# Performance work log

Hardware: AMD Instinct MI355X
Metric: run time of the kernel (lower is better)

## Reference

```python
import jax, jax.numpy as jnp
import numpy as np

N = 20000      # nodes
E = 200000     # edges
IN = 128       # in_feat
OUT = 128      # out_feat
NB = 8         # num_bases
SI = IN // NB  # submat_in = 16
SO = OUT // NB # submat_out = 16
R = 230        # num_rels
T = 365        # total_times


def setup_inputs() -> dict:
    key = jax.random.key(0)
    ks = jax.random.split(key, 11)
    h = jax.random.normal(ks[0], (N, IN), jnp.float32)
    edge_norm = jax.random.uniform(ks[1], (E, 1), jnp.float32)
    node_norm = jax.random.uniform(ks[2], (N, 1), jnp.float32)
    weight = jax.random.normal(ks[3], (R, NB * SI * SO), jnp.float32) * 0.05
    h_bias = jnp.zeros((OUT,), jnp.float32)
    loop_weight = jax.random.normal(ks[4], (IN, OUT), jnp.float32) * 0.05
    time_embed = jax.random.normal(ks[5], (T, IN), jnp.float32) * 0.05
    edge_src = jax.random.randint(ks[6], (E,), 0, N)
    edge_dst = jax.random.randint(ks[7], (E,), 0, N)
    edge_type = jax.random.randint(ks[8], (E,), 0, R)
    time_idx = jax.random.randint(ks[9], (N,), 0, T)
    return dict(h=h, edge_norm=edge_norm, node_norm=node_norm, weight=weight,
                h_bias=h_bias, loop_weight=loop_weight, time_embed=time_embed,
                edge_src=edge_src, edge_dst=edge_dst, edge_type=edge_type,
                time_idx=time_idx)


def reference(h, edge_norm, node_norm, weight, h_bias, loop_weight, time_embed,
              edge_src, edge_dst, edge_type, time_idx):
    # self-loop message
    loop_message = h @ loop_weight                              # [N, OUT]
    # msg_func: per-edge relation weight gather + block-diagonal bmm
    W_e = weight[edge_type].reshape(-1, NB, SI, SO)             # [E, NB, SI, SO]
    src = h[edge_src].reshape(-1, NB, SI)                       # [E, NB, SI]
    msg = jnp.einsum('ebi,ebio->ebo', src, W_e).reshape(-1, OUT)  # [E, OUT]
    msg = msg * edge_norm
    # fn.sum aggregation over destination nodes
    agg = jax.ops.segment_sum(msg, edge_dst, num_segments=N)    # [N, OUT]
    # apply_func: scale by node norm, then bias + self loop + activation
    node_repr = agg * node_norm
    node_repr = node_repr + h_bias + loop_message
    node_repr = jax.nn.relu(node_repr)
    # get_time_embedding: per-node time embedding gather
    time_embedding = time_embed[time_idx]                       # [N, IN]
    return node_repr, time_embedding
```

## Files before the change

kernel.cpp:

```cpp
#include <hip/hip_runtime.h>

#define N 20000
#define E 200000
#define IN 128
#define OUT 128
#define NB 8
#define SI 16
#define SO 16
#define R 230
#define T 365

__device__ float  g_W_t[(size_t)R * NB * SO * SI];
__device__ ushort g_msg[(size_t)E * OUT];
__device__ int    g_cnt_d[N];
__device__ int    g_off_d[N];
__device__ int    g_cur_d[N];
__device__ int    g_cnt_r[R * 16];
__device__ int    g_cur_r[R * 16];
__device__ int    g_pos[E];
__device__ int    g_eid_r[E];
__device__ int    g_total_d;
__device__ int    g_total_r;

__device__ __forceinline__ ushort f2bf(float f) {
    unsigned u = __float_as_uint(f);
    return (ushort)((u + 0x7fffu + ((u >> 16) & 1u)) >> 16);
}
__device__ __forceinline__ float bf2f(ushort v) {
    return __uint_as_float((unsigned)v << 16);
}

__global__ __launch_bounds__(256) void hist_kernel(
        const float* __restrict__ weight,
        const int* __restrict__ edge_dst,
        const int* __restrict__ edge_type) {
    __shared__ int lh[R];
    const int tid  = threadIdx.x;
    const int gtid = blockIdx.x * 256 + tid;
    for (int t = gtid; t < R * NB * SI * SO; t += gridDim.x * 256) {
        int r  = t >> 11;
        int b  = (t >> 8) & 7;
        int ol = (t >> 4) & 15;
        int i  = t & 15;
        g_W_t[t] = weight[(long)r * 2048 + b * 256 + i * 16 + ol];
    }
    for (int j = tid; j < R; j += 256) lh[j] = 0;
    __syncthreads();
    for (long e = gtid; e < E; e += (long)gridDim.x * 256) {
        atomicAdd(&g_cnt_d[edge_dst[e]], 1);
        atomicAdd(&lh[edge_type[e]], 1);
    }
    __syncthreads();
    for (int j = tid; j < R; j += 256)
        if (lh[j]) atomicAdd(&g_cnt_r[j * 16], lh[j]);
}

__global__ __launch_bounds__(256) void alloc_kernel() {
    int idx  = blockIdx.x * blockDim.x + threadIdx.x;
    int lane = threadIdx.x & 63;
    const int NPAD = 20032;
    if (idx < NPAD) {
        int c = (idx < N) ? g_cnt_d[idx] : 0;
        int x = c;
        for (int d = 1; d < 64; d <<= 1) {
            int y = __shfl_up(x, d);
            if (lane >= d) x += y;
        }
        int base = 0;
        if (lane == 63) base = atomicAdd(&g_total_d, x);
        base = __shfl(base, 63);
        if (idx < N) {
            int off = base + x - c;
            g_off_d[idx] = off;
            g_cur_d[idx] = off;
        }
    } else if (idx < NPAD + 256) {
        int j = idx - NPAD;
        int c = (j < R) ? g_cnt_r[j * 16] : 0;
        int x = c;
        for (int d = 1; d < 64; d <<= 1) {
            int y = __shfl_up(x, d);
            if (lane >= d) x += y;
        }
        int base = 0;
        if (lane == 63) base = atomicAdd(&g_total_r, x);
        base = __shfl(base, 63);
        if (j < R) g_cur_r[j * 16] = base + x - c;
    }
}

__global__ void scatter_kernel(const int* __restrict__ edge_dst,
                               const int* __restrict__ edge_type) {
    int e = blockIdx.x * blockDim.x + threadIdx.x;
    if (e < E) {
        g_pos[e] = atomicAdd(&g_cur_d[edge_dst[e]], 1);
        int pr = atomicAdd(&g_cur_r[edge_type[e] * 16], 1);
        g_eid_r[pr] = e;
    }
}

__global__ __launch_bounds__(256) void msg_kernel(
        const float* __restrict__ h,
        const float* __restrict__ edge_norm,
        const int* __restrict__ edge_src,
        const int* __restrict__ edge_type) {
    __shared__ __attribute__((aligned(16))) float hsm[32 * 132];
    __shared__ int   ssrc[32], stype[32], spos[32];
    __shared__ float snorm[32];

    const int tid = threadIdx.x;
    const int lo  = blockIdx.x * 32;

    if (tid < 32) {
        int e = g_eid_r[lo + tid];
        ssrc[tid]  = edge_src[e];
        stype[tid] = edge_type[e];
        snorm[tid] = edge_norm[e];
        spos[tid]  = g_pos[e];
    }
    __syncthreads();

    {
        const int row = tid >> 3;
        const int c0  = (tid & 7) * 4;
        const float* hp = h + (long)ssrc[row] * IN;
        float* dst = &hsm[row * 132];
#pragma unroll
        for (int j = 0; j < 4; ++j) {
            float4 v = *reinterpret_cast<const float4*>(hp + c0 + 32 * j);
            *reinterpret_cast<float4*>(dst + c0 + 32 * j) = v;
        }
    }
    __syncthreads();

    const int slot = tid >> 7;
    const int o    = tid & 127;
    const int b    = o >> 4;
    const int ol   = o & 15;

#define MSG_BODY(K, W0, W1, W2, W3)                                          \
    {                                                                        \
        const float* hrow = &hsm[(K) * 132 + b * 16];                        \
        float4 h0 = *reinterpret_cast<const float4*>(hrow);                  \
        float4 h1 = *reinterpret_cast<const float4*>(hrow + 4);              \
        float4 h2 = *reinterpret_cast<const float4*>(hrow + 8);              \
        float4 h3 = *reinterpret_cast<const float4*>(hrow + 12);             \
        float m0 = 0.f, m1 = 0.f;                                            \
        m0 = fmaf(h0.x, W0.x, m0); m0 = fmaf(h0.y, W0.y, m0);                \
        m0 = fmaf(h0.z, W0.z, m0); m0 = fmaf(h0.w, W0.w, m0);                \
        m1 = fmaf(h1.x, W1.x, m1); m1 = fmaf(h1.y, W1.y, m1);                \
        m1 = fmaf(h1.z, W1.z, m1); m1 = fmaf(h1.w, W1.w, m1);                \
        m0 = fmaf(h2.x, W2.x, m0); m0 = fmaf(h2.y, W2.y, m0);                \
        m0 = fmaf(h2.z, W2.z, m0); m0 = fmaf(h2.w, W2.w, m0);                \
        m1 = fmaf(h3.x, W3.x, m1); m1 = fmaf(h3.y, W3.y, m1);                \
        m1 = fmaf(h3.z, W3.z, m1); m1 = fmaf(h3.w, W3.w, m1);                \
        __builtin_nontemporal_store(f2bf(snorm[K] * (m0 + m1)),              \
                                    &g_msg[(long)spos[K] * OUT + o]);        \
    }

    if (stype[0] == stype[31]) {
        const float4* wp = reinterpret_cast<const float4*>(
            g_W_t + (long)stype[0] * 2048 + b * 256 + ol * 16);
        float4 w0 = wp[0], w1 = wp[1], w2 = wp[2], w3 = wp[3];
#pragma unroll 4
        for (int k = slot; k < 32; k += 2)
            MSG_BODY(k, w0, w1, w2, w3)
    } else {
        int rcur = -1;
        float4 w0, w1, w2, w3;
        for (int k = slot; k < 32; k += 2) {
            int r = stype[k];
            if (r != rcur) {
                const float4* wp = reinterpret_cast<const float4*>(
                    g_W_t + (long)r * 2048 + b * 256 + ol * 16);
                w0 = wp[0]; w1 = wp[1]; w2 = wp[2]; w3 = wp[3];
                rcur = r;
            }
            MSG_BODY(k, w0, w1, w2, w3)
        }
    }
#undef MSG_BODY
}

__global__ __launch_bounds__(128) void node_kernel(
        const float* __restrict__ h,
        const float* __restrict__ node_norm,
        const float* __restrict__ h_bias,
        const float* __restrict__ loop_weight,
        const float* __restrict__ time_embed,
        const int* __restrict__ time_idx,
        float* __restrict__ out) {
    __shared__ float hsm[IN * 8];
    const int o    = threadIdx.x;
    const int base = blockIdx.x * 8;

    for (int k = o; k < 8 * IN; k += 128) {
        int nl = k >> 7;
        int i  = k & 127;
        hsm[i * 8 + nl] = h[(long)(base + nl) * IN + i];
    }
    __syncthreads();

    float acc[8];
#pragma unroll
    for (int nl = 0; nl < 8; ++nl) {
        int n  = base + nl;
        int st = g_off_d[n];
        int cn = g_cnt_d[n];
        float a0 = 0.f, a1 = 0.f, a2 = 0.f, a3 = 0.f;
        const ushort* mp = g_msg + (long)st * OUT + o;
        int k = 0;
        for (; k + 3 < cn; k += 4) {
            a0 += bf2f(__builtin_nontemporal_load(&mp[(long)(k + 0) * OUT]));
            a1 += bf2f(__builtin_nontemporal_load(&mp[(long)(k + 1) * OUT]));
            a2 += bf2f(__builtin_nontemporal_load(&mp[(long)(k + 2) * OUT]));
            a3 += bf2f(__builtin_nontemporal_load(&mp[(long)(k + 3) * OUT]));
        }
        for (; k < cn; ++k)
            a0 += bf2f(__builtin_nontemporal_load(&mp[(long)k * OUT]));
        acc[nl] = ((a0 + a1) + (a2 + a3)) * node_norm[n];
    }

    float sl[8];
#pragma unroll
    for (int nl = 0; nl < 8; ++nl) sl[nl] = 0.f;

    for (int i0 = 0; i0 < IN; i0 += 8) {
        float w[8];
#pragma unroll
        for (int j = 0; j < 8; ++j)
            w[j] = loop_weight[(long)(i0 + j) * OUT + o];
#pragma unroll
        for (int j = 0; j < 8; ++j) {
            const float* row = &hsm[(i0 + j) * 8];
            float4 p0 = *reinterpret_cast<const float4*>(row);
            float4 p1 = *reinterpret_cast<const float4*>(row + 4);
            sl[0] = fmaf(p0.x, w[j], sl[0]); sl[1] = fmaf(p0.y, w[j], sl[1]);
            sl[2] = fmaf(p0.z, w[j], sl[2]); sl[3] = fmaf(p0.w, w[j], sl[3]);
            sl[4] = fmaf(p1.x, w[j], sl[4]); sl[5] = fmaf(p1.y, w[j], sl[5]);
            sl[6] = fmaf(p1.z, w[j], sl[6]); sl[7] = fmaf(p1.w, w[j], sl[7]);
        }
    }

    const float bias = h_bias[o];
#pragma unroll
    for (int nl = 0; nl < 8; ++nl) {
        int n = base + nl;
        float v = acc[nl] + bias + sl[nl];
        out[(long)n * OUT + o] = fmaxf(v, 0.f);
        out[(long)N * OUT + (long)n * IN + o] =
            time_embed[(long)time_idx[n] * IN + o];
    }

    __syncthreads();
    if (o < 8) g_cnt_d[base + o] = 0;
    {
        int j = blockIdx.x * 128 + o;
        if (j < R * 16) g_cnt_r[j] = 0;
    }
    if (blockIdx.x == 0 && o == 0) { g_total_d = 0; g_total_r = 0; }
}

extern "C" void kernel_launch(void* const* d_in, const int* in_sizes, int n_in,
                              void* d_out, int out_size, void* d_ws, size_t ws_size,
                              hipStream_t stream) {
    const float* h           = (const float*)d_in[0];
    const float* edge_norm   = (const float*)d_in[1];
    const float* node_norm   = (const float*)d_in[2];
    const float* weight      = (const float*)d_in[3];
    const float* h_bias      = (const float*)d_in[4];
    const float* loop_weight = (const float*)d_in[5];
    const float* time_embed  = (const float*)d_in[6];
    const int*   edge_src    = (const int*)d_in[7];
    const int*   edge_dst    = (const int*)d_in[8];
    const int*   edge_type   = (const int*)d_in[9];
    const int*   time_idx    = (const int*)d_in[10];
    float* out = (float*)d_out;

    hist_kernel<<<400, 256, 0, stream>>>(weight, edge_dst, edge_type);
    alloc_kernel<<<80, 256, 0, stream>>>();
    scatter_kernel<<<(E + 255) / 256, 256, 0, stream>>>(edge_dst, edge_type);
    msg_kernel<<<E / 32, 256, 0, stream>>>(h, edge_norm, edge_src, edge_type);
    node_kernel<<<N / 8, 128, 0, stream>>>(h, node_norm, h_bias, loop_weight,
                                           time_embed, time_idx, out);
}
```

Baseline: 229.5 us.

## Fuse prefix-scan into histogram kernel via last-block pattern; widen node kernel loads

Merges the alloc kernel into the histogram kernel: the last block to finish, detected with an atomic counter and fences, performs the prefix scans over destination and relation counts, which removes one launch. The node kernel is restructured so each thread handles two output columns, reading bf16 message pairs as 32-bit words and loop_weight as float2. It also reads h rows directly instead of staging them in shared memory, processing 16 nodes per 256-thread block. The serial scan of 20000 counts in a single block may lengthen the critical path, and the g_done counter now has to be reset in the node kernel.

```diff
diff --git a/kernel.cpp b/kernel.cpp
--- a/kernel.cpp
+++ b/kernel.cpp
@@ -21,6 +21,7 @@
 __device__ int    g_eid_r[E];
 __device__ int    g_total_d;
 __device__ int    g_total_r;
+__device__ unsigned g_done;
 
 __device__ __forceinline__ ushort f2bf(float f) {
     unsigned u = __float_as_uint(f);
@@ -29,15 +30,24 @@
 __device__ __forceinline__ float bf2f(ushort v) {
     return __uint_as_float((unsigned)v << 16);
 }
-
-__global__ __launch_bounds__(256) void hist_kernel(
+__device__ __forceinline__ float bflo(unsigned m) {
+    return __uint_as_float(m << 16);
+}
+__device__ __forceinline__ float bfhi(unsigned m) {
+    return __uint_as_float(m & 0xffff0000u);
+}
+
+__global__ __launch_bounds__(256) void build_kernel(
         const float* __restrict__ weight,
         const int* __restrict__ edge_dst,
         const int* __restrict__ edge_type) {
     __shared__ int lh[R];
+    __shared__ int s_last;
     const int tid  = threadIdx.x;
     const int gtid = blockIdx.x * 256 + tid;
-    for (int t = gtid; t < R * NB * SI * SO; t += gridDim.x * 256) {
+    const int GSZ  = gridDim.x * 256;
+
+    for (int t = gtid; t < R * NB * SI * SO; t += GSZ) {
         int r  = t >> 11;
         int b  = (t >> 8) & 7;
         int ol = (t >> 4) & 15;
@@ -46,46 +56,55 @@
     }
     for (int j = tid; j < R; j += 256) lh[j] = 0;
     __syncthreads();
-    for (long e = gtid; e < E; e += (long)gridDim.x * 256) {
+    for (int e = gtid; e < E; e += GSZ) {
         atomicAdd(&g_cnt_d[edge_dst[e]], 1);
         atomicAdd(&lh[edge_type[e]], 1);
     }
     __syncthreads();
     for (int j = tid; j < R; j += 256)
         if (lh[j]) atomicAdd(&g_cnt_r[j * 16], lh[j]);
-}
-
-__global__ __launch_bounds__(256) void alloc_kernel() {
-    int idx  = blockIdx.x * blockDim.x + threadIdx.x;
-    int lane = threadIdx.x & 63;
-    const int NPAD = 20032;
-    if (idx < NPAD) {
-        int c = (idx < N) ? g_cnt_d[idx] : 0;
+
+    __syncthreads();
+    if (tid == 0) {
+        __threadfence();
+        unsigned d = atomicAdd(&g_done, 1u);
+        s_last = (d == (unsigned)(gridDim.x - 1)) ? 1 : 0;
+    }
+    __syncthreads();
+    if (!s_last) return;
+    __threadfence();
+
+    const int lane = tid & 63;
+    for (int idx = tid; idx < 20032; idx += 256) {
+        int c = (idx < N) ? __hip_atomic_load(&g_cnt_d[idx], __ATOMIC_RELAXED,
+                                              __HIP_MEMORY_SCOPE_AGENT) : 0;
         int x = c;
         for (int d = 1; d < 64; d <<= 1) {
             int y = __shfl_up(x, d);
             if (lane >= d) x += y;
         }
-        int base = 0;
-        if (lane == 63) base = atomicAdd(&g_total_d, x);
-        base = __shfl(base, 63);
+        int bse = 0;
+        if (lane == 63) bse = atomicAdd(&g_total_d, x);
+        bse = __shfl(bse, 63);
         if (idx < N) {
-            int off = base + x - c;
+            int off = bse + x - c;
             g_off_d[idx] = off;
             g_cur_d[idx] = off;
         }
-    } else if (idx < NPAD + 256) {
-        int j = idx - NPAD;
-        int c = (j < R) ? g_cnt_r[j * 16] : 0;
+    }
+    {
+        int j = tid;
+        int c = (j < R) ? __hip_atomic_load(&g_cnt_r[j * 16], __ATOMIC_RELAXED,
+                                            __HIP_MEMORY_SCOPE_AGENT) : 0;
         int x = c;
         for (int d = 1; d < 64; d <<= 1) {
             int y = __shfl_up(x, d);
             if (lane >= d) x += y;
         }
-        int base = 0;
-        if (lane == 63) base = atomicAdd(&g_total_r, x);
-        base = __shfl(base, 63);
-        if (j < R) g_cur_r[j * 16] = base + x - c;
+        int bse = 0;
+        if (lane == 63) bse = atomicAdd(&g_total_r, x);
+        bse = __shfl(bse, 63);
+        if (j < R) g_cur_r[j * 16] = bse + x - c;
     }
 }
 
@@ -182,7 +201,7 @@
 #undef MSG_BODY
 }
 
-__global__ __launch_bounds__(128) void node_kernel(
+__global__ __launch_bounds__(256) void node_kernel(
         const float* __restrict__ h,
         const float* __restrict__ node_norm,
         const float* __restrict__ h_bias,
@@ -190,75 +209,101 @@
         const float* __restrict__ time_embed,
         const int* __restrict__ time_idx,
         float* __restrict__ out) {
-    __shared__ float hsm[IN * 8];
-    const int o    = threadIdx.x;
-    const int base = blockIdx.x * 8;
-
-    for (int k = o; k < 8 * IN; k += 128) {
-        int nl = k >> 7;
-        int i  = k & 127;
-        hsm[i * 8 + nl] = h[(long)(base + nl) * IN + i];
-    }
-    __syncthreads();
-
-    float acc[8];
+    const int t    = threadIdx.x;
+    const int q    = t & 63;
+    const int grp  = t >> 6;
+    const int base = blockIdx.x * 16 + grp * 4;
+
+    const unsigned* msg32 = reinterpret_cast<const unsigned*>(g_msg);
+
+    float accL[4], accH[4];
 #pragma unroll
-    for (int nl = 0; nl < 8; ++nl) {
-        int n  = base + nl;
-        int st = g_off_d[n];
-        int cn = g_cnt_d[n];
-        float a0 = 0.f, a1 = 0.f, a2 = 0.f, a3 = 0.f;
-        const ushort* mp = g_msg + (long)st * OUT + o;
+    for (int nl = 0; nl < 4; ++nl) {
+        const int n  = base + nl;
+        const int st = g_off_d[n];
+        const int cn = g_cnt_d[n];
+        const unsigned* mp = msg32 + (size_t)st * 64 + q;
+        float aL0 = 0.f, aL1 = 0.f, aH0 = 0.f, aH1 = 0.f;
         int k = 0;
         for (; k + 3 < cn; k += 4) {
-            a0 += bf2f(__builtin_nontemporal_load(&mp[(long)(k + 0) * OUT]));
-            a1 += bf2f(__builtin_nontemporal_load(&mp[(long)(k + 1) * OUT]));
-            a2 += bf2f(__builtin_nontemporal_load(&mp[(long)(k + 2) * OUT]));
-            a3 += bf2f(__builtin_nontemporal_load(&mp[(long)(k + 3) * OUT]));
-        }
-        for (; k < cn; ++k)
-            a0 += bf2f(__builtin_nontemporal_load(&mp[(long)k * OUT]));
-        acc[nl] = ((a0 + a1) + (a2 + a3)) * node_norm[n];
-    }
-
-    float sl[8];
+            unsigned m0 = __builtin_nontemporal_load(mp + (size_t)(k + 0) * 64);
+            unsigned m1 = __builtin_nontemporal_load(mp + (size_t)(k + 1) * 64);
+            unsigned m2 = __builtin_nontemporal_load(mp + (size_t)(k + 2) * 64);
+            unsigned m3 = __builtin_nontemporal_load(mp + (size_t)(k + 3) * 64);
+            aL0 += bflo(m0); aH0 += bfhi(m0);
+            aL1 += bflo(m1); aH1 += bfhi(m1);
+            aL0 += bflo(m2); aH0 += bfhi(m2);
+            aL1 += bflo(m3); aH1 += bfhi(m3);
+        }
+        for (; k < cn; ++k) {
+            unsigned m = __builtin_nontemporal_load(mp + (size_t)k * 64);
+            aL0 += bflo(m); aH0 += bfhi(m);
+        }
+        float nn = node_norm[n];
+        accL[nl] = (aL0 + aL1) * nn;
+        accH[nl] = (aH0 + aH1) * nn;
+    }
+
+    float slL0 = 0.f, slL1 = 0.f, slL2 = 0.f, slL3 = 0.f;
+    float slH0 = 0.f, slH1 = 0.f, slH2 = 0.f, slH3 = 0.f;
+    const float2* lw2 = reinterpret_cast<const float2*>(loop_weight);
+    const float* hp0 = h + (size_t)(base + 0) * IN;
+    const float* hp1 = h + (size_t)(base + 1) * IN;
+    const float* hp2 = h + (size_t)(base + 2) * IN;
+    const float* hp3 = h + (size_t)(base + 3) * IN;
+#pragma unroll 4
+    for (int i0 = 0; i0 < IN; i0 += 4) {
+        float2 w0 = lw2[(size_t)(i0 + 0) * 64 + q];
+        float2 w1 = lw2[(size_t)(i0 + 1) * 64 + q];
+        float2 w2 = lw2[(size_t)(i0 + 2) * 64 + q];
+        float2 w3 = lw2[(size_t)(i0 + 3) * 64 + q];
+        float4 v0 = *reinterpret_cast<const float4*>(hp0 + i0);
+        float4 v1 = *reinterpret_cast<const float4*>(hp1 + i0);
+        float4 v2 = *reinterpret_cast<const float4*>(hp2 + i0);
+        float4 v3 = *reinterpret_cast<const float4*>(hp3 + i0);
+        slL0 = fmaf(v0.x, w0.x, slL0); slL0 = fmaf(v0.y, w1.x, slL0);
+        slL0 = fmaf(v0.z, w2.x, slL0); slL0 = fmaf(v0.w, w3.x, slL0);
+        slH0 = fmaf(v0.x, w0.y, slH0); slH0 = fmaf(v0.y, w1.y, slH0);
+        slH0 = fmaf(v0.z, w2.y, slH0); slH0 = fmaf(v0.w, w3.y, slH0);
+        slL1 = fmaf(v1.x, w0.x, slL1); slL1 = fmaf(v1.y, w1.x, slL1);
+        slL1 = fmaf(v1.z, w2.x, slL1); slL1 = fmaf(v1.w, w3.x, slL1);
+        slH1 = fmaf(v1.x, w0.y, slH1); slH1 = fmaf(v1.y, w1.y, slH1);
+        slH1 = fmaf(v1.z, w2.y, slH1); slH1 = fmaf(v1.w, w3.y, slH1);
+        slL2 = fmaf(v2.x, w0.x, slL2); slL2 = fmaf(v2.y, w1.x, slL2);
+        slL2 = fmaf(v2.z, w2.x, slL2); slL2 = fmaf(v2.w, w3.x, slL2);
+        slH2 = fmaf(v2.x, w0.y, slH2); slH2 = fmaf(v2.y, w1.y, slH2);
+        slH2 = fmaf(v2.z, w2.y, slH2); slH2 = fmaf(v2.w, w3.y, slH2);
+        slL3 = fmaf(v3.x, w0.x, slL3); slL3 = fmaf(v3.y, w1.x, slL3);
+        slL3 = fmaf(v3.z, w2.x, slL3); slL3 = fmaf(v3.w, w3.x, slL3);
+        slH3 = fmaf(v3.x, w0.y, slH3); slH3 = fmaf(v3.y, w1.y, slH3);
+        slH3 = fmaf(v3.z, w2.y, slH3); slH3 = fmaf(v3.w, w3.y, slH3);
+    }
+    float slL[4] = {slL0, slL1, slL2, slL3};
+    float slH[4] = {slH0, slH1, slH2, slH3};
+
+    const float2 bias = reinterpret_cast<const float2*>(h_bias)[q];
+    float2* o2  = reinterpret_cast<float2*>(out);
+    float2* o2b = reinterpret_cast<float2*>(out + (size_t)N * OUT);
+    const float2* te2 = reinterpret_cast<const float2*>(time_embed);
 #pragma unroll
-    for (int nl = 0; nl < 8; ++nl) sl[nl] = 0.f;
-
-    for (int i0 = 0; i0 < IN; i0 += 8) {
-        float w[8];
-#pragma unroll
-        for (int j = 0; j < 8; ++j)
-            w[j] = loop_weight[(long)(i0 + j) * OUT + o];
-#pragma unroll
-        for (int j = 0; j < 8; ++j) {
-            const float* row = &hsm[(i0 + j) * 8];
-            float4 p0 = *reinterpret_cast<const float4*>(row);
-            float4 p1 = *reinterpret_cast<const float4*>(row + 4);
-            sl[0] = fmaf(p0.x, w[j], sl[0]); sl[1] = fmaf(p0.y, w[j], sl[1]);
-            sl[2] = fmaf(p0.z, w[j], sl[2]); sl[3] = fmaf(p0.w, w[j], sl[3]);
-            sl[4] = fmaf(p1.x, w[j], sl[4]); sl[5] = fmaf(p1.y, w[j], sl[5]);
-            sl[6] = fmaf(p1.z, w[j], sl[6]); sl[7] = fmaf(p1.w, w[j], sl[7]);
-        }
-    }
-
-    const float bias = h_bias[o];
-#pragma unroll
-    for (int nl = 0; nl < 8; ++nl) {
-        int n = base + nl;
-        float v = acc[nl] + bias + sl[nl];
-        out[(long)n * OUT + o] = fmaxf(v, 0.f);
-        out[(long)N * OUT + (long)n * IN + o] =
-            time_embed[(long)time_idx[n] * IN + o];
-    }
-
-    __syncthreads();
-    if (o < 8) g_cnt_d[base + o] = 0;
+    for (int nl = 0; nl < 4; ++nl) {
+        const int n = base + nl;
+        float2 v;
+        v.x = fmaxf(accL[nl] + bias.x + slL[nl], 0.f);
+        v.y = fmaxf(accH[nl] + bias.y + slH[nl], 0.f);
+        o2[(size_t)n * 64 + q] = v;
+        o2b[(size_t)n * 64 + q] = te2[(size_t)time_idx[n] * 64 + q];
+    }
+
+    __syncthreads();
+    if (t < 16) g_cnt_d[blockIdx.x * 16 + t] = 0;
     {
-        int j = blockIdx.x * 128 + o;
+        int j = blockIdx.x * 256 + t;
         if (j < R * 16) g_cnt_r[j] = 0;
     }
-    if (blockIdx.x == 0 && o == 0) { g_total_d = 0; g_total_r = 0; }
+    if (blockIdx.x == 0 && t == 0) {
+        g_total_d = 0; g_total_r = 0; g_done = 0u;
+    }
 }
 
 extern "C" void kernel_launch(void* const* d_in, const int* in_sizes, int n_in,
@@ -277,10 +322,9 @@
     const int*   time_idx    = (const int*)d_in[10];
     float* out = (float*)d_out;
 
-    hist_kernel<<<400, 256, 0, stream>>>(weight, edge_dst, edge_type);
-    alloc_kernel<<<80, 256, 0, stream>>>();
+    build_kernel<<<400, 256, 0, stream>>>(weight, edge_dst, edge_type);
     scatter_kernel<<<(E + 255) / 256, 256, 0, stream>>>(edge_dst, edge_type);
     msg_kernel<<<E / 32, 256, 0, stream>>>(h, edge_norm, edge_src, edge_type);
-    node_kernel<<<N / 8, 128, 0, stream>>>(h, node_norm, h_bias, loop_weight,
-                                           time_embed, time_idx, out);
-}
+    node_kernel<<<N / 16, 256, 0, stream>>>(h, node_norm, h_bias, loop_weight,
+                                            time_embed, time_idx, out);
+}
```

Measured after the change: 298.3 us. 30.0% more time.
